# Kernel tuning notes

Measured on AMD Instinct MI355X. Metric: run time of the kernel, lower is better.

The kernel has to match this reference:

```python
import jax, jax.numpy as jnp
import numpy as np

B, N, D = 2, 2048, 768
H = 12
HD = D // H  # 64

def setup_inputs() -> dict:
    key = jax.random.key(0)
    ks = jax.random.split(key, 5)
    scale = 1.0 / np.sqrt(D)
    return {
        "x": jax.random.normal(ks[0], (B, N, D), dtype=jnp.float32),
        "W_kqv": jax.random.normal(ks[1], (H, 3 * HD, D), dtype=jnp.float32) * scale,
        "b_kqv": jax.random.normal(ks[2], (H, 3 * HD), dtype=jnp.float32) * 0.01,
        "W_proj": jax.random.normal(ks[3], (D, D), dtype=jnp.float32) * scale,
        "b_proj": jax.random.normal(ks[4], (D,), dtype=jnp.float32) * 0.01,
    }

def reference(x, W_kqv, b_kqv, W_proj, b_proj):
    # Per-head Linear: x @ W_h^T + b_h, all heads at once -> [B, H, N, 3*HD]
    kqv = jnp.einsum('bnd,hod->bhno', x, W_kqv) + b_kqv[None, :, None, :]
    k, q, v = jnp.split(kqv, 3, axis=-1)  # each [B, H, N, HD]
    # scores = q @ k^T / sqrt(head_dim)  (attention_scores(a=k, b=q))
    scores = jnp.einsum('bhqd,bhkd->bhqk', q, k) / jnp.sqrt(jnp.asarray(HD, x.dtype))
    # causal mask (tril): masked_fill with -inf where mask == 0
    causal = jnp.tril(jnp.ones((N, N), dtype=bool))
    scores = jnp.where(causal[None, None, :, :], scores, -jnp.inf)
    attn = jax.nn.softmax(scores, axis=-1)
    sa = jnp.einsum('bhqk,bhkd->bhqd', attn, v)  # [B, H, N, HD]
    # concat heads along feature dim (head order preserved)
    sa = sa.transpose(0, 2, 1, 3).reshape(B, N, D)
    # output projection
    return sa @ W_proj.T + b_proj
```

## Files before the change

### kernel.cpp

```cpp
#include <hip/hip_runtime.h>

#define BB 2
#define SEQ 2048
#define DIM 768
#define NH 12
#define HD 64

typedef _Float16 half8 __attribute__((ext_vector_type(8)));
typedef float floatx4 __attribute__((ext_vector_type(4)));

__device__ __forceinline__ void gl_lds16(const _Float16* g, _Float16* l) {
    __builtin_amdgcn_global_load_lds(
        (const __attribute__((address_space(1))) void*)g,
        (__attribute__((address_space(3))) void*)l, 16, 0, 0);
}

__global__ __launch_bounds__(256)
void cvt3(const float* __restrict__ s0, _Float16* __restrict__ d0, int nb0,
          const float* __restrict__ s1, _Float16* __restrict__ d1, int nb1,
          const float* __restrict__ s2, _Float16* __restrict__ d2) {
    int b = blockIdx.x;
    const float* s; _Float16* d;
    if (b < nb0)            { s = s0; d = d0; }
    else if (b < nb0 + nb1) { s = s1; d = d1; b -= nb0; }
    else                    { s = s2; d = d2; b -= nb0 + nb1; }
    const int i = (b * 256 + threadIdx.x) * 8;
    float4 a = *(const float4*)(s + i);
    float4 c = *(const float4*)(s + i + 4);
    half8 h;
    h[0] = (_Float16)a.x; h[1] = (_Float16)a.y; h[2] = (_Float16)a.z; h[3] = (_Float16)a.w;
    h[4] = (_Float16)c.x; h[5] = (_Float16)c.y; h[6] = (_Float16)c.z; h[7] = (_Float16)c.w;
    *(half8*)(d + i) = h;
}

#define GEMM_CORE(APTR, BPTR)                                                   \
    __shared__ _Float16 Asl[2][128 * 32];                                       \
    __shared__ _Float16 Bsl[2][128 * 32];                                       \
    const int t = threadIdx.x, w = t >> 6, lane = t & 63;                       \
    const int quad = lane >> 4, l15 = lane & 15;                                \
    const int wm = w >> 1, wn = w & 1;                                          \
    const int m0 = blockIdx.y * 128, c0 = blockIdx.x * 128;                     \
    const floatx4 z4 = {0.f, 0.f, 0.f, 0.f};                                    \
    floatx4 acc[4][4];                                                          \
    _Pragma("unroll") for (int i = 0; i < 4; ++i)                               \
        _Pragma("unroll") for (int j = 0; j < 4; ++j) acc[i][j] = z4;           \
    const _Float16* pA = APTR + (size_t)(m0 + w * 32 + l15) * DIM + quad * 8;   \
    const _Float16* pB = BPTR + (size_t)(c0 + w * 32 + l15) * DIM + quad * 8;   \
    gl_lds16(pA,            &Asl[0][(w * 2 + 0) * 512]);                        \
    gl_lds16(pA + 16 * DIM, &Asl[0][(w * 2 + 1) * 512]);                        \
    gl_lds16(pB,            &Bsl[0][(w * 2 + 0) * 512]);                        \
    gl_lds16(pB + 16 * DIM, &Bsl[0][(w * 2 + 1) * 512]);                        \
    for (int k0 = 0, it = 0; k0 < DIM; k0 += 32, ++it) {                        \
        const int buf = it & 1;                                                 \
        __syncthreads();                                                        \
        if (k0 + 32 < DIM) {                                                    \
            gl_lds16(pA + k0 + 32,            &Asl[buf ^ 1][(w * 2 + 0) * 512]);\
            gl_lds16(pA + k0 + 32 + 16 * DIM, &Asl[buf ^ 1][(w * 2 + 1) * 512]);\
            gl_lds16(pB + k0 + 32,            &Bsl[buf ^ 1][(w * 2 + 0) * 512]);\
            gl_lds16(pB + k0 + 32 + 16 * DIM, &Bsl[buf ^ 1][(w * 2 + 1) * 512]);\
        }                                                                       \
        half8 af[4], bf[4];                                                     \
        _Pragma("unroll") for (int i = 0; i < 4; ++i)                           \
            af[i] = *(const half8*)&Asl[buf][(wm * 4 + i) * 512 + lane * 8];    \
        _Pragma("unroll") for (int j = 0; j < 4; ++j)                           \
            bf[j] = *(const half8*)&Bsl[buf][(wn * 4 + j) * 512 + lane * 8];    \
        _Pragma("unroll") for (int i = 0; i < 4; ++i)                           \
            _Pragma("unroll") for (int j = 0; j < 4; ++j)                       \
                acc[i][j] = __builtin_amdgcn_mfma_f32_16x16x32_f16(             \
                    af[i], bf[j], acc[i][j], 0, 0, 0);                          \
    }

__global__ __launch_bounds__(256)
void kqv_gemm2(const _Float16* __restrict__ xh, const _Float16* __restrict__ Wh,
               const float* __restrict__ bias, _Float16* __restrict__ kb,
               _Float16* __restrict__ qb, _Float16* __restrict__ vb) {
    GEMM_CORE(xh, Wh)
    #pragma unroll
    for (int j = 0; j < 4; ++j) {
        const int cbase = c0 + (wn * 4 + j) * 16;
        const int h = cbase / 192;
        const int rem = cbase - h * 192;
        const int part = rem >> 6;
        const int d = (rem & 63) + l15;
        _Float16* dst = (part == 0) ? kb : (part == 1 ? qb : vb);
        const float bv = bias[cbase + l15];
        #pragma unroll
        for (int i = 0; i < 4; ++i)
            #pragma unroll
            for (int r = 0; r < 4; ++r) {
                const int m = m0 + (wm * 4 + i) * 16 + quad * 4 + r;
                const int bidx = m >> 11, n = m & (SEQ - 1);
                dst[(((size_t)(bidx * NH + h) * SEQ + n) << 6) + d] =
                    (_Float16)(acc[i][j][r] + bv);
            }
    }
}

__global__ __launch_bounds__(256)
void proj_gemm3(const _Float16* __restrict__ A, const _Float16* __restrict__ Wh,
                const float* __restrict__ bias, float* __restrict__ out) {
    __shared__ _Float16 Asl[2][128 * 32];
    __shared__ _Float16 Bsl[2][64 * 32];
    const int t = threadIdx.x, w = t >> 6, lane = t & 63;
    const int quad = lane >> 4, l15 = lane & 15;
    const int wm = w >> 1, wn = w & 1;
    const int m0 = blockIdx.y * 128, c0 = blockIdx.x * 64;
    const floatx4 z4 = {0.f, 0.f, 0.f, 0.f};
    floatx4 acc[4][2];
    #pragma unroll
    for (int i = 0; i < 4; ++i)
        #pragma unroll
        for (int j = 0; j < 2; ++j) acc[i][j] = z4;
    const _Float16* pA = A  + (size_t)(m0 + w * 32 + l15) * DIM + quad * 8;
    const _Float16* pB = Wh + (size_t)(c0 + w * 16 + l15) * DIM + quad * 8;
    gl_lds16(pA,            &Asl[0][(w * 2 + 0) * 512]);
    gl_lds16(pA + 16 * DIM, &Asl[0][(w * 2 + 1) * 512]);
    gl_lds16(pB,            &Bsl[0][w * 512]);
    for (int k0 = 0, it = 0; k0 < DIM; k0 += 32, ++it) {
        const int buf = it & 1;
        __syncthreads();
        if (k0 + 32 < DIM) {
            gl_lds16(pA + k0 + 32,            &Asl[buf ^ 1][(w * 2 + 0) * 512]);
            gl_lds16(pA + k0 + 32 + 16 * DIM, &Asl[buf ^ 1][(w * 2 + 1) * 512]);
            gl_lds16(pB + k0 + 32,            &Bsl[buf ^ 1][w * 512]);
        }
        half8 af[4], bf[2];
        #pragma unroll
        for (int i = 0; i < 4; ++i)
            af[i] = *(const half8*)&Asl[buf][(wm * 4 + i) * 512 + lane * 8];
        #pragma unroll
        for (int j = 0; j < 2; ++j)
            bf[j] = *(const half8*)&Bsl[buf][(wn * 2 + j) * 512 + lane * 8];
        #pragma unroll
        for (int i = 0; i < 4; ++i)
            #pragma unroll
            for (int j = 0; j < 2; ++j)
                acc[i][j] = __builtin_amdgcn_mfma_f32_16x16x32_f16(
                    af[i], bf[j], acc[i][j], 0, 0, 0);
    }
    #pragma unroll
    for (int j = 0; j < 2; ++j) {
        const int cbase = c0 + (wn * 2 + j) * 16;
        const float bv = bias[cbase + l15];
        #pragma unroll
        for (int i = 0; i < 4; ++i)
            #pragma unroll
            for (int r = 0; r < 4; ++r) {
                const int m = m0 + (wm * 4 + i) * 16 + quad * 4 + r;
                out[(size_t)m * DIM + cbase + l15] = acc[i][j][r] + bv;
            }
    }
}

__global__ __launch_bounds__(256)
void v_transpose(const _Float16* __restrict__ vb, _Float16* __restrict__ vbT) {
    __shared__ _Float16 T[64 * 72];
    const int t = threadIdx.x;
    const int s0 = blockIdx.x * 64;
    const size_t base = (size_t)blockIdx.y * (SEQ * HD);
    {
        const int s = t >> 2, doff = (t & 3) * 16;
        const _Float16* src = vb + base + (size_t)(s0 + s) * HD + doff;
        *(half8*)&T[s * 72 + doff]     = *(const half8*)src;
        *(half8*)&T[s * 72 + doff + 8] = *(const half8*)(src + 8);
    }
    __syncthreads();
    {
        const int d = t >> 2, soff = (t & 3) * 16;
        half8 o0, o1;
        #pragma unroll
        for (int k = 0; k < 8; ++k) o0[k] = T[(soff + k) * 72 + d];
        #pragma unroll
        for (int k = 0; k < 8; ++k) o1[k] = T[(soff + 8 + k) * 72 + d];
        _Float16* dst = vbT + base + (size_t)d * SEQ + s0 + soff;
        *(half8*)dst       = o0;
        *(half8*)(dst + 8) = o1;
    }
}

__global__ __launch_bounds__(256)
void attn_mfma(const _Float16* __restrict__ qb, const _Float16* __restrict__ kbuf,
               const _Float16* __restrict__ vbT, _Float16* __restrict__ sa,
               _Float16* __restrict__ Opart, float* __restrict__ lpart) {
    __shared__ _Float16 Kl[2][64 * 64];
    __shared__ _Float16 Vl[2][64 * 64];
    __shared__ _Float16 Pl[8][16 * 64];
    int u = 39 - blockIdx.x, q, p, np;
    if (u < 4)       { q = u;               p = 0;     np = 1; }
    else if (u < 12) { int v = u - 4;  q = 4  + (v >> 1); p = v & 1; np = 2; }
    else if (u < 24) { int v = u - 12; q = 8  + v / 3;    p = v % 3; np = 3; }
    else             { int v = u - 24; q = 12 + (v >> 2); p = v & 3; np = 4; }
    const int ntiles = 2 * q + 2;
    const int kt0 = p * 8;
    const int ktn = (p == np - 1) ? (ntiles - kt0) : 8;

    const int bh = blockIdx.y;
    const int t = threadIdx.x, w = t >> 6, lane = t & 63, quad = lane >> 4, l15 = lane & 15;
    const size_t base = (size_t)bh * (SEQ * HD);
    const int i0 = q * 128 + w * 32;
    const _Float16* Kg = kbuf + base;
    const _Float16* Vg = vbT + base;

    const int lr = lane >> 3, gg = lane & 7;
    const int gs = (gg ^ (lr & 7)) * 8;

    half8 aq[2][2];
    const _Float16 qs = (_Float16)(0.125f * 1.44269504f);
    #pragma unroll
    for (int rt = 0; rt < 2; ++rt)
        #pragma unroll
        for (int ks = 0; ks < 2; ++ks) {
            aq[rt][ks] = *(const half8*)(qb + base +
                          (size_t)(i0 + rt * 16 + l15) * HD + ks * 32 + quad * 8);
            #pragma unroll
            for (int k = 0; k < 8; ++k) aq[rt][ks][k] *= qs;
        }

    const floatx4 z4 = {0.f, 0.f, 0.f, 0.f};
    floatx4 O[2][4];
    float l_part[2][4];
    #pragma unroll
    for (int rt = 0; rt < 2; ++rt)
        #pragma unroll
        for (int k = 0; k < 4; ++k) { O[rt][k] = z4; l_part[rt][k] = 0.f; }

    #pragma unroll
    for (int pp = 0; pp < 2; ++pp) {
        const int c = w * 2 + pp, row = c * 8 + lr;
        gl_lds16(Kg + (size_t)(kt0 * 64 + row) * HD + gs,  &Kl[0][c * 512]);
        gl_lds16(Vg + (size_t)row * SEQ + kt0 * 64 + gs,   &Vl[0][c * 512]);
    }

    const int swz = l15 & 7;
    const int prow = quad * 4;

    for (int it = 0; it < ktn; ++it) {
        const int kt = kt0 + it;
        const int buf = it & 1;
        const int j0 = kt * 64;
        __syncthreads();

        if (it + 1 < ktn) {
            const _Float16* Kn = Kg + (size_t)(j0 + 64) * HD;
            const _Float16* Vn = Vg + (j0 + 64);
            #pragma unroll
            for (int pp = 0; pp < 2; ++pp) {
                const int c = w * 2 + pp, row = c * 8 + lr;
                gl_lds16(Kn + (size_t)row * HD + gs,  &Kl[buf ^ 1][c * 512]);
                gl_lds16(Vn + (size_t)row * SEQ + gs, &Vl[buf ^ 1][c * 512]);
            }
        }
        if (j0 > i0 + 31) continue;

        floatx4 S[2][4];
        #pragma unroll
        for (int rt = 0; rt < 2; ++rt)
            #pragma unroll
            for (int nt = 0; nt < 4; ++nt) S[rt][nt] = z4;
        #pragma unroll
        for (int ks = 0; ks < 2; ++ks)
            #pragma unroll
            for (int nt = 0; nt < 4; ++nt) {
                half8 bk = *(const half8*)&Kl[buf][(nt * 16 + l15) * 64 +
                                                   (((ks * 4 + quad) ^ swz) << 3)];
                S[0][nt] = __builtin_amdgcn_mfma_f32_16x16x32_f16(aq[0][ks], bk, S[0][nt], 0, 0, 0);
                S[1][nt] = __builtin_amdgcn_mfma_f32_16x16x32_f16(aq[1][ks], bk, S[1][nt], 0, 0, 0);
            }

        asm volatile("" ::: "memory");
        if (j0 + 63 > i0) {
            #pragma unroll
            for (int rt = 0; rt < 2; ++rt)
                #pragma unroll
                for (int nt = 0; nt < 4; ++nt) {
                    const int j = j0 + nt * 16 + l15;
                    #pragma unroll
                    for (int r = 0; r < 4; ++r) {
                        float pv = exp2f(S[rt][nt][r]);
                        if (j > (i0 + rt * 16 + prow + r)) pv = 0.f;
                        l_part[rt][r] += pv;
                        const int row = prow + r, col = nt * 16 + l15;
                        Pl[w * 2 + rt][row * 64 + (((col >> 3) ^ (row & 7)) << 3) + (col & 7)] =
                            (_Float16)pv;
                    }
                }
        } else {
            #pragma unroll
            for (int rt = 0; rt < 2; ++rt)
                #pragma unroll
                for (int nt = 0; nt < 4; ++nt)
                    #pragma unroll
                    for (int r = 0; r < 4; ++r) {
                        float pv = exp2f(S[rt][nt][r]);
                        l_part[rt][r] += pv;
                        const int row = prow + r, col = nt * 16 + l15;
                        Pl[w * 2 + rt][row * 64 + (((col >> 3) ^ (row & 7)) << 3) + (col & 7)] =
                            (_Float16)pv;
                    }
        }
        asm volatile("" ::: "memory");
        #pragma unroll
        for (int ks = 0; ks < 2; ++ks) {
            half8 ap0 = *(const half8*)&Pl[w * 2 + 0][l15 * 64 + (((ks * 4 + quad) ^ swz) << 3)];
            half8 ap1 = *(const half8*)&Pl[w * 2 + 1][l15 * 64 + (((ks * 4 + quad) ^ swz) << 3)];
            #pragma unroll
            for (int dt = 0; dt < 4; ++dt) {
                half8 bv = *(const half8*)&Vl[buf][(dt * 16 + l15) * 64 +
                                                    (((ks * 4 + quad) ^ swz) << 3)];
                O[0][dt] = __builtin_amdgcn_mfma_f32_16x16x32_f16(ap0, bv, O[0][dt], 0, 0, 0);
                O[1][dt] = __builtin_amdgcn_mfma_f32_16x16x32_f16(ap1, bv, O[1][dt], 0, 0, 0);
            }
        }
    }

    if (np == 1) {
        const int bidx = bh / NH, h = bh - bidx * NH;
        #pragma unroll
        for (int rt = 0; rt < 2; ++rt)
            #pragma unroll
            for (int r = 0; r < 4; ++r) {
                float rs = l_part[rt][r];
                #pragma unroll
                for (int off = 1; off < 16; off <<= 1) rs += __shfl_xor(rs, off);
                const float inv = 1.0f / rs;
                const int i = i0 + rt * 16 + quad * 4 + r;
                #pragma unroll
                for (int dt = 0; dt < 4; ++dt)
                    sa[(size_t)(bidx * SEQ + i) * DIM + h * HD + dt * 16 + l15] =
                        (_Float16)(O[rt][dt][r] * inv);
            }
    } else {
        const size_t slot = ((size_t)(bh * 16 + q) * 4 + p);
        _Float16* Od = Opart + slot * 8192;
        float*    ld = lpart + slot * 128;
        #pragma unroll
        for (int rt = 0; rt < 2; ++rt)
            #pragma unroll
            for (int r = 0; r < 4; ++r) {
                float rs = l_part[rt][r];
                #pragma unroll
                for (int off = 1; off < 16; off <<= 1) rs += __shfl_xor(rs, off);
                const int row = w * 32 + rt * 16 + quad * 4 + r;
                ld[row] = rs;
                #pragma unroll
                for (int dt = 0; dt < 4; ++dt)
                    Od[row * 64 + dt * 16 + l15] = (_Float16)O[rt][dt][r];
            }
    }
}

__global__ __launch_bounds__(256)
void attn_combine(const _Float16* __restrict__ Opart, const float* __restrict__ lpart,
                  _Float16* __restrict__ sa) {
    const int q = 4 + blockIdx.x;
    const int bh = blockIdx.y;
    const int np = (q < 8) ? 2 : (q < 12 ? 3 : 4);
    const int t = threadIdx.x;
    const int row = t >> 1, d0 = (t & 1) * 32;
    const size_t slot0 = (size_t)(bh * 16 + q) * 4;

    float lsum = 0.f;
    for (int p = 0; p < np; ++p) lsum += lpart[(slot0 + p) * 128 + row];

    float acc[32];
    #pragma unroll
    for (int k = 0; k < 32; ++k) acc[k] = 0.f;
    for (int p = 0; p < np; ++p) {
        const _Float16* src = Opart + (slot0 + p) * 8192 + row * 64 + d0;
        #pragma unroll
        for (int v = 0; v < 4; ++v) {
            half8 a = *(const half8*)(src + v * 8);
            #pragma unroll
            for (int k = 0; k < 8; ++k) acc[v * 8 + k] += (float)a[k];
        }
    }
    const float inv = 1.0f / lsum;
    const int bidx = bh / NH, h = bh - bidx * NH;
    _Float16* dst = sa + (size_t)(bidx * SEQ + q * 128 + row) * DIM + h * HD + d0;
    #pragma unroll
    for (int v = 0; v < 4; ++v) {
        half8 o;
        #pragma unroll
        for (int k = 0; k < 8; ++k) o[k] = (_Float16)(acc[v * 8 + k] * inv);
        *(half8*)(dst + v * 8) = o;
    }
}

extern "C" void kernel_launch(void* const* d_in, const int* in_sizes, int n_in,
                              void* d_out, int out_size, void* d_ws, size_t ws_size,
                              hipStream_t stream) {
    (void)in_sizes; (void)n_in; (void)out_size; (void)ws_size;
    const float* x  = (const float*)d_in[0];
    const float* Wk = (const float*)d_in[1];
    const float* bk = (const float*)d_in[2];
    const float* Wp = (const float*)d_in[3];
    const float* bp = (const float*)d_in[4];
    float* out = (float*)d_out;

    _Float16* ws = (_Float16*)d_ws;
    const size_t per = (size_t)BB * NH * SEQ * HD;
    const int nx = BB * SEQ * DIM;
    const int nwk = NH * 3 * HD * DIM;
    const int nwp = DIM * DIM;
    _Float16* kb  = ws;
    _Float16* qb  = ws + per;
    _Float16* vb  = ws + 2 * per;
    _Float16* vbT = ws + 3 * per;
    _Float16* sa  = ws + 4 * per;
    _Float16* xh  = ws + 5 * per;
    _Float16* Wkh = xh + nx;
    _Float16* Wph = Wkh + nwk;
    _Float16* Opart = Wph + nwp;
    float*    lpart = (float*)(Opart + (size_t)24 * 16 * 4 * 8192);

    const int nb0 = nx / 2048, nb1 = nwk / 2048, nb2 = nwp / 2048;
    cvt3<<<dim3(nb0 + nb1 + nb2), 256, 0, stream>>>(x, xh, nb0, Wk, Wkh, nb1, Wp, Wph);

    kqv_gemm2  <<<dim3(18, 32), 256, 0, stream>>>(xh, Wkh, bk, kb, qb, vb);
    v_transpose<<<dim3(32, 24), 256, 0, stream>>>(vb, vbT);
    attn_mfma  <<<dim3(40, 24), 256, 0, stream>>>(qb, kb, vbT, sa, Opart, lpart);
    attn_combine<<<dim3(12, 24), 256, 0, stream>>>(Opart, lpart, sa);
    proj_gemm3 <<<dim3(12, 32), 256, 0, stream>>>(sa, Wph, bp, out);
}
```

Baseline: 188.8 us.

## Transpose S MFMA, pack P stores, compute row sums via MFMA with ones

Swaps the MFMA operands for QK^T so each lane holds four consecutive key columns of one query row. P can then be written to LDS as packed half4 values converted with cvt_pkrtz, instead of one scalar half store per element. Row sums are accumulated by an extra MFMA against a vector of ones, which removes the per-row shuffle reductions. The change also halves the P scratch buffer to one tile per wave, preloads V fragments into registers, and processes the two row tiles one after another. In exchange it adds extra MFMA work and more register pressure, and the row sums are now taken from fp16-rounded P.

Measured after the change: 189.6 us. No clear change (+0.4%).

```diff
diff --git a/kernel.cpp b/kernel.cpp
--- a/kernel.cpp
+++ b/kernel.cpp
@@ -7,6 +7,7 @@
 #define HD 64
 
 typedef _Float16 half8 __attribute__((ext_vector_type(8)));
+typedef _Float16 half4 __attribute__((ext_vector_type(4)));
 typedef float floatx4 __attribute__((ext_vector_type(4)));
 
 __device__ __forceinline__ void gl_lds16(const _Float16* g, _Float16* l) {
@@ -184,7 +185,7 @@
                _Float16* __restrict__ Opart, float* __restrict__ lpart) {
     __shared__ _Float16 Kl[2][64 * 64];
     __shared__ _Float16 Vl[2][64 * 64];
-    __shared__ _Float16 Pl[8][16 * 64];
+    __shared__ _Float16 Pl[4][16 * 64];
     int u = 39 - blockIdx.x, q, p, np;
     if (u < 4)       { q = u;               p = 0;     np = 1; }
     else if (u < 12) { int v = u - 4;  q = 4  + (v >> 1); p = v & 1; np = 2; }
@@ -198,6 +199,7 @@
     const int t = threadIdx.x, w = t >> 6, lane = t & 63, quad = lane >> 4, l15 = lane & 15;
     const size_t base = (size_t)bh * (SEQ * HD);
     const int i0 = q * 128 + w * 32;
+    _Float16* Pw = Pl[w];
     const _Float16* Kg = kbuf + base;
     const _Float16* Vg = vbT + base;
 
@@ -216,13 +218,18 @@
             for (int k = 0; k < 8; ++k) aq[rt][ks][k] *= qs;
         }
 
+    half8 ones;
+    #pragma unroll
+    for (int k = 0; k < 8; ++k) ones[k] = (_Float16)1.0f;
+
     const floatx4 z4 = {0.f, 0.f, 0.f, 0.f};
-    floatx4 O[2][4];
-    float l_part[2][4];
-    #pragma unroll
-    for (int rt = 0; rt < 2; ++rt)
-        #pragma unroll
-        for (int k = 0; k < 4; ++k) { O[rt][k] = z4; l_part[rt][k] = 0.f; }
+    floatx4 O[2][4], l_acc[2];
+    #pragma unroll
+    for (int rt = 0; rt < 2; ++rt) {
+        l_acc[rt] = z4;
+        #pragma unroll
+        for (int k = 0; k < 4; ++k) O[rt][k] = z4;
+    }
 
     #pragma unroll
     for (int pp = 0; pp < 2; ++pp) {
@@ -232,7 +239,8 @@
     }
 
     const int swz = l15 & 7;
-    const int prow = quad * 4;
+    const int pmask = (l15 & 7) << 1;
+    const int prbase = l15 * 64;
 
     for (int it = 0; it < ktn; ++it) {
         const int kt = kt0 + it;
@@ -263,52 +271,56 @@
             for (int nt = 0; nt < 4; ++nt) {
                 half8 bk = *(const half8*)&Kl[buf][(nt * 16 + l15) * 64 +
                                                    (((ks * 4 + quad) ^ swz) << 3)];
-                S[0][nt] = __builtin_amdgcn_mfma_f32_16x16x32_f16(aq[0][ks], bk, S[0][nt], 0, 0, 0);
-                S[1][nt] = __builtin_amdgcn_mfma_f32_16x16x32_f16(aq[1][ks], bk, S[1][nt], 0, 0, 0);
-            }
-
-        asm volatile("" ::: "memory");
-        if (j0 + 63 > i0) {
-            #pragma unroll
-            for (int rt = 0; rt < 2; ++rt)
-                #pragma unroll
-                for (int nt = 0; nt < 4; ++nt) {
-                    const int j = j0 + nt * 16 + l15;
+                S[0][nt] = __builtin_amdgcn_mfma_f32_16x16x32_f16(bk, aq[0][ks], S[0][nt], 0, 0, 0);
+                S[1][nt] = __builtin_amdgcn_mfma_f32_16x16x32_f16(bk, aq[1][ks], S[1][nt], 0, 0, 0);
+            }
+
+        half8 bvr[2][4];
+        #pragma unroll
+        for (int ks = 0; ks < 2; ++ks)
+            #pragma unroll
+            for (int dt = 0; dt < 4; ++dt)
+                bvr[ks][dt] = *(const half8*)&Vl[buf][(dt * 16 + l15) * 64 +
+                                                      (((ks * 4 + quad) ^ swz) << 3)];
+
+        const bool masked = (j0 + 63 > i0);
+        #pragma unroll
+        for (int rt = 0; rt < 2; ++rt) {
+            asm volatile("" ::: "memory");
+            const int iq = i0 + rt * 16 + l15;
+            #pragma unroll
+            for (int nt = 0; nt < 4; ++nt) {
+                float pv[4];
+                if (masked) {
+                    const int jb = j0 + nt * 16 + quad * 4;
                     #pragma unroll
                     for (int r = 0; r < 4; ++r) {
-                        float pv = exp2f(S[rt][nt][r]);
-                        if (j > (i0 + rt * 16 + prow + r)) pv = 0.f;
-                        l_part[rt][r] += pv;
-                        const int row = prow + r, col = nt * 16 + l15;
-                        Pl[w * 2 + rt][row * 64 + (((col >> 3) ^ (row & 7)) << 3) + (col & 7)] =
-                            (_Float16)pv;
+                        float e = exp2f(S[rt][nt][r]);
+                        pv[r] = (jb + r > iq) ? 0.f : e;
                     }
+                } else {
+                    #pragma unroll
+                    for (int r = 0; r < 4; ++r) pv[r] = exp2f(S[rt][nt][r]);
                 }
-        } else {
-            #pragma unroll
-            for (int rt = 0; rt < 2; ++rt)
+                auto lo = __builtin_amdgcn_cvt_pkrtz(pv[0], pv[1]);
+                auto hi = __builtin_amdgcn_cvt_pkrtz(pv[2], pv[3]);
+                half4 pk;
+                pk[0] = (_Float16)lo[0]; pk[1] = (_Float16)lo[1];
+                pk[2] = (_Float16)hi[0]; pk[3] = (_Float16)hi[1];
+                const int slot = (nt * 4 + quad) ^ pmask;
+                *(half4*)&Pw[prbase + slot * 4] = pk;
+            }
+            asm volatile("" ::: "memory");
+            #pragma unroll
+            for (int ks = 0; ks < 2; ++ks) {
+                const int rslot = (ks * 8 + quad * 2) ^ pmask;
+                half8 ap = *(const half8*)&Pw[prbase + rslot * 4];
                 #pragma unroll
-                for (int nt = 0; nt < 4; ++nt)
-                    #pragma unroll
-                    for (int r = 0; r < 4; ++r) {
-                        float pv = exp2f(S[rt][nt][r]);
-                        l_part[rt][r] += pv;
-                        const int row = prow + r, col = nt * 16 + l15;
-                        Pl[w * 2 + rt][row * 64 + (((col >> 3) ^ (row & 7)) << 3) + (col & 7)] =
-                            (_Float16)pv;
-                    }
-        }
-        asm volatile("" ::: "memory");
-        #pragma unroll
-        for (int ks = 0; ks < 2; ++ks) {
-            half8 ap0 = *(const half8*)&Pl[w * 2 + 0][l15 * 64 + (((ks * 4 + quad) ^ swz) << 3)];
-            half8 ap1 = *(const half8*)&Pl[w * 2 + 1][l15 * 64 + (((ks * 4 + quad) ^ swz) << 3)];
-            #pragma unroll
-            for (int dt = 0; dt < 4; ++dt) {
-                half8 bv = *(const half8*)&Vl[buf][(dt * 16 + l15) * 64 +
-                                                    (((ks * 4 + quad) ^ swz) << 3)];
-                O[0][dt] = __builtin_amdgcn_mfma_f32_16x16x32_f16(ap0, bv, O[0][dt], 0, 0, 0);
-                O[1][dt] = __builtin_amdgcn_mfma_f32_16x16x32_f16(ap1, bv, O[1][dt], 0, 0, 0);
+                for (int dt = 0; dt < 4; ++dt)
+                    O[rt][dt] = __builtin_amdgcn_mfma_f32_16x16x32_f16(
+                        ap, bvr[ks][dt], O[rt][dt], 0, 0, 0);
+                l_acc[rt] = __builtin_amdgcn_mfma_f32_16x16x32_f16(
+                    ap, ones, l_acc[rt], 0, 0, 0);
             }
         }
     }
@@ -319,10 +331,7 @@
         for (int rt = 0; rt < 2; ++rt)
             #pragma unroll
             for (int r = 0; r < 4; ++r) {
-                float rs = l_part[rt][r];
-                #pragma unroll
-                for (int off = 1; off < 16; off <<= 1) rs += __shfl_xor(rs, off);
-                const float inv = 1.0f / rs;
+                const float inv = 1.0f / l_acc[rt][r];
                 const int i = i0 + rt * 16 + quad * 4 + r;
                 #pragma unroll
                 for (int dt = 0; dt < 4; ++dt)
@@ -337,11 +346,8 @@
         for (int rt = 0; rt < 2; ++rt)
             #pragma unroll
             for (int r = 0; r < 4; ++r) {
-                float rs = l_part[rt][r];
-                #pragma unroll
-                for (int off = 1; off < 16; off <<= 1) rs += __shfl_xor(rs, off);
                 const int row = w * 32 + rt * 16 + quad * 4 + r;
-                ld[row] = rs;
+                ld[row] = l_acc[rt][r];
                 #pragma unroll
                 for (int dt = 0; dt < 4; ++dt)
                     Od[row * 64 + dt * 16 + l15] = (_Float16)O[rt][dt][r];
```
